# Performance work log

Hardware: AMD Instinct MI355X
Metric: run time of the kernel (lower is better)

The kernel has to match this reference:

```python
import jax, jax.numpy as jnp
import numpy as np

KERNEL_SIZE = 3


def extract_local_features(feature_map, point_coords, kernel_size=KERNEL_SIZE):
    # feature_map: (B,C,H,W); point_coords: (B,N,2) normalized (y,x) in [0,1]
    B, C, H, W = feature_map.shape
    half = kernel_size // 2
    x = (point_coords[..., 1] * (W - 1)).astype(jnp.int32)  # (B,N)
    y = (point_coords[..., 0] * (H - 1)).astype(jnp.int32)
    x_min = jnp.clip(x - half, 0, None)
    x_max = jnp.clip(x + half + 1, None, W)
    y_min = jnp.clip(y - half, 0, None)
    y_max = jnpp_clip = jnp.clip(y + half + 1, None, H)
    y_max = jnp.clip(y + half + 1, None, H)
    # gather a fixed (k,k) window with clamped offsets, mask out-of-window entries
    offs = jnp.arange(kernel_size)  # (k,)
    yy = y_min[..., None] + offs  # (B,N,k) candidate rows
    xx = x_min[..., None] + offs  # (B,N,k)
    y_valid = yy < y_max[..., None]
    x_valid = xx < x_max[..., None]
    yy_c = jnp.clip(yy, 0, H - 1)
    xx_c = jnp.clip(xx, 0, W - 1)
    # flat spatial indices (B,N,k,k)
    flat_idx = yy_c[..., :, None] * W + xx_c[..., None, :]
    valid = (y_valid[..., :, None] & x_valid[..., None, :]).astype(feature_map.dtype)
    fm_flat = feature_map.reshape(B, C, H * W)  # (B,C,HW)

    def per_batch(fm, idx, val):
        # fm: (C,HW); idx,val: (N,k,k)
        g = fm[:, idx.reshape(-1)].reshape(fm.shape[0], *idx.shape)  # (C,N,k,k)
        s = jnp.einsum('cnij,nij->cn', g, val)
        cnt = val.sum(axis=(-1, -2))  # (N,)
        return s / cnt[None, :]

    return jax.vmap(per_batch)(fm_flat, flat_idx, valid)  # (B,C,N)


def point_sample(inp, point_coords):
    # bilinear grid_sample, align_corners=False, coords in [0,1] as (x,y) order
    # per the code: grid = 2*coords - 1; grid_sample uses (x,y) convention
    B, C, H, W = inp.shape
    gx = point_coords[..., 0]  # (B,N) in [0,1]
    gy = point_coords[..., 1]
    # align_corners=False mapping: pix = ((g*2-1)+1)/2 * size - 0.5 = g*size - 0.5
    fx = gx * W - 0.5
    fy = gy * H - 0.5
    x0 = jnp.floor(fx).astype(jnp.int32)
    y0 = jnp.floor(fy).astype(jnp.int32)
    wx = fx - x0
    wy = fy - y0

    def gather(yc, xc):
        inb = ((yc >= 0) & (yc < H) & (xc >= 0) & (xc < W)).astype(inp.dtype)  # (B,N)
        ycc = jnp.clip(yc, 0, H - 1)
        xcc = jnp.clip(xc, 0, W - 1)
        flat = ycc * W + xcc  # (B,N)
        fm = inp.reshape(B, C, H * W)
        g = jax.vmap(lambda f, i: f[:, i])(fm, flat)  # (B,C,N)
        return g * inb[:, None, :]

    v00 = gather(y0, x0)
    v01 = gather(y0, x0 + 1)
    v10 = gather(y0 + 1, x0)
    v11 = gather(y0 + 1, x0 + 1)
    wx_ = wx[:, None, :]
    wy_ = wy[:, None, :]
    out = (v00 * (1 - wx_) * (1 - wy_) + v01 * wx_ * (1 - wy_)
           + v10 * (1 - wx_) * wy_ + v11 * wx_ * wy_)  # (B,C,N)
    return out.transpose(0, 2, 1)  # (B,N,C)


def calculate_uncertainty(mask_logits):
    return -jnp.abs(mask_logits).squeeze(1)  # (B,H,W)


def edge_topk_sampling(edge_masks, uncertainty_map, topk):
    # edge_masks: (B,H,W) {0,1}; uncertainty_map: (B,H,W)
    B, H, W = edge_masks.shape
    NEG = jnp.asarray(-1e30, uncertainty_map.dtype)
    masked_u = jnp.where(edge_masks.reshape(B, -1) == 1,
                         uncertainty_map.reshape(B, -1), NEG)
    vals, idx = jax.lax.top_k(masked_u, topk)  # (B,topk)
    yi = (idx // W).astype(jnp.float32)
    xi = (idx % W).astype(jnp.float32)
    coords = jnp.stack([yi / (H - 1), xi / (W - 1)], axis=-1)  # (B,topk,2) (y,x)
    return idx, coords


def setup_inputs() -> dict:
    key = jax.random.key(0)
    k1, k2, k3, k4 = jax.random.split(key, 4)
    B, C, H, W = 8, 256, 256, 256
    N = 4096
    feature_map = jax.random.normal(k1, (B, C, H, W), dtype=jnp.float32)
    pred_mask = jax.random.normal(k2, (B, 1, H, W), dtype=jnp.float32)
    edge_masks = jax.random.randint(k3, (B, H, W), 0, 2).astype(jnp.int32)
    point_coords = jax.random.uniform(k4, (B, N, 2), dtype=jnp.float32)
    return {"feature_map": feature_map, "pred_mask": pred_mask,
            "edge_masks": edge_masks, "point_coords": point_coords,
            "topk": 4096}


def reference(feature_map, pred_mask, edge_masks, point_coords, topk):
    uncertainty_map = calculate_uncertainty(pred_mask)  # (B,H,W)
    idx, important_coords = edge_topk_sampling(edge_masks, uncertainty_map, topk)
    local_feats = extract_local_features(feature_map, important_coords)  # (B,C,topk)
    sampled = point_sample(feature_map, point_coords)  # (B,N,C)
    return local_feats, sampled, important_coords, idx
```

## Files before the change

### kernel.cpp

```cpp
#include <hip/hip_runtime.h>

#define CC 256
#define HH 256
#define WW 256
#define HWV 65536
#define NN 4096

using u64 = unsigned long long;
using u32 = unsigned int;

__global__ void build_keys_k(const float* __restrict__ pm, const int* __restrict__ em,
                             u64* __restrict__ keys) {
    int i = blockIdx.x * blockDim.x + threadIdx.x;
    float f = (em[i] == 1) ? -fabsf(pm[i]) : -1e30f;
    u32 u = __float_as_uint(f);
    u32 k = (u & 0x80000000u) ? ~u : (u | 0x80000000u);
    u32 pix = (u32)i & 0xFFFFu;
    keys[i] = ((u64)k << 16) | (u64)(0xFFFFu - pix);
}

__global__ __launch_bounds__(1024) void topk_sortpc_k(const u64* __restrict__ keys,
                                                      const float* __restrict__ pc,
                                                      u32* __restrict__ stash,
                                                      u32* __restrict__ pixSorted,
                                                      u32* __restrict__ pcSorted) {
    __shared__ u64 sel[NN];
    __shared__ u64 bm[1024];
    __shared__ u32 wp[1024];
    __shared__ u32 s_digit, s_rem, s_cnt;
    const int t = threadIdx.x;
    if (blockIdx.x < 8) {
        const int b = blockIdx.x;
        const u64* kb = keys + (size_t)b * HWV;
        u32* hist = (u32*)sel;
        u64 prefix = 0ULL;
        u32 remaining = NN;
        for (int r = 0; r < 4; ++r) {
            int shift = 36 - 12 * r;
            #pragma unroll
            for (int q = 0; q < 4; ++q) hist[t + q * 1024] = 0u;
            __syncthreads();
            for (int i = t; i < HWV; i += 1024) {
                u64 K = kb[i];
                if ((K >> (shift + 12)) == prefix)
                    atomicAdd(&hist[(u32)((K >> shift) & 0xFFFULL)], 1u);
            }
            __syncthreads();
            for (int off = 1; off < 4096; off <<= 1) {
                u32 v[4];
                #pragma unroll
                for (int q = 0; q < 4; ++q) {
                    int i = t + q * 1024;
                    v[q] = hist[i];
                    if (i + off < 4096) v[q] += hist[i + off];
                }
                __syncthreads();
                #pragma unroll
                for (int q = 0; q < 4; ++q) hist[t + q * 1024] = v[q];
                __syncthreads();
            }
            #pragma unroll
            for (int q = 0; q < 4; ++q) {
                int d = t + q * 1024;
                u32 ge = hist[d];
                u32 gt = (d < 4095) ? hist[d + 1] : 0u;
                if (ge >= remaining && gt < remaining) { s_digit = (u32)d; s_rem = remaining - gt; }
            }
            __syncthreads();
            prefix = (prefix << 12) | (u64)s_digit;
            remaining = s_rem;
            __syncthreads();
        }
        if (t == 0) s_cnt = 0u;
        __syncthreads();
        for (int i = t; i < HWV; i += 1024) {
            u64 K = kb[i];
            if (K >= prefix) { u32 p = atomicAdd(&s_cnt, 1u); sel[p] = K; }
        }
        __syncthreads();
        for (int k = 2; k <= NN; k <<= 1) {
            for (int j = k >> 1; j > 0; j >>= 1) {
                for (int i = t; i < NN; i += 1024) {
                    int l = i ^ j;
                    if (l > i) {
                        u64 a = sel[i], c = sel[l];
                        bool asc = ((i & k) == 0);
                        if ((a < c) == asc) { sel[i] = c; sel[l] = a; }
                    }
                }
                __syncthreads();
            }
        }
        bm[t] = 0ULL;
        __syncthreads();
        #pragma unroll
        for (int q = 0; q < 4; ++q) {
            int r = t + q * 1024;
            u32 pix = 0xFFFFu - (u32)(sel[r] & 0xFFFFULL);
            stash[b * NN + r] = pix;
            atomicOr(&bm[pix >> 6], 1ULL << (pix & 63));
        }
        __syncthreads();
        wp[t] = (u32)__popcll(bm[t]);
        __syncthreads();
        for (int off = 1; off < 1024; off <<= 1) {
            u32 v = wp[t];
            if (t >= off) v += wp[t - off];
            __syncthreads();
            wp[t] = v;
            __syncthreads();
        }
        #pragma unroll
        for (int q = 0; q < 4; ++q) {
            int r = t + q * 1024;
            u32 pix = 0xFFFFu - (u32)(sel[r] & 0xFFFFULL);
            int w = (int)(pix >> 6);
            u32 pos = wp[w] - (u32)__popcll(bm[w])
                    + (u32)__popcll(bm[w] & ((1ULL << (pix & 63)) - 1ULL));
            pixSorted[b * NN + pos] = (pix << 12) | (u32)r;
        }
    } else {
        const int b = blockIdx.x - 8;
        u32* cellArr = (u32*)sel;
        u32* hist256 = wp;
        u32* cnt     = (u32*)bm;
        if (t < 256) { hist256[t] = 0u; cnt[t] = 0u; }
        __syncthreads();
        for (int n = t; n < NN; n += 1024) {
            float gx = pc[((size_t)b * NN + n) * 2 + 0];
            float gy = pc[((size_t)b * NN + n) * 2 + 1];
            float fx = gx * 256.0f - 0.5f;
            float fy = gy * 256.0f - 0.5f;
            int x0 = (int)floorf(fx), y0 = (int)floorf(fy);
            int xc = min(max(x0, 0), 255), yc = min(max(y0, 0), 255);
            cellArr[n] = ((u32)(yc * 256 + xc) << 12) | (u32)n;
            atomicAdd(&hist256[yc], 1u);
        }
        __syncthreads();
        for (int off = 1; off < 256; off <<= 1) {
            u32 v = 0;
            if (t < 256) { v = hist256[t]; if (t >= off) v += hist256[t - off]; }
            __syncthreads();
            if (t < 256) hist256[t] = v;
            __syncthreads();
        }
        for (int n = t; n < NN; n += 1024) {
            u32 pk = cellArr[n];
            u32 yc = pk >> 20;
            u32 base = (yc > 0) ? hist256[yc - 1] : 0u;
            u32 pos = base + atomicAdd(&cnt[yc], 1u);
            pcSorted[b * NN + pos] = pk;
        }
    }
}

template<int MODE>
__global__ __launch_bounds__(256) void gather_k(const float* __restrict__ fm,
                                                const float* __restrict__ pc,
                                                const u32* __restrict__ pixSorted,
                                                const u32* __restrict__ pcSorted,
                                                float* __restrict__ outLp,
                                                float* __restrict__ outS) {
    __shared__ float tile[256][33];
    __shared__ u32 pidx[256];
    const int b = blockIdx.z, j0 = blockIdx.x * 256, t = threadIdx.x;
    bool doL; int c0;
    if (MODE == 0) { doL = (blockIdx.y < 8); c0 = (doL ? blockIdx.y : blockIdx.y - 8) * 32; }
    else if (MODE == 1) { doL = true; c0 = blockIdx.y * 32; }
    else { doL = false; c0 = blockIdx.y * 32; }
    const float* planes = fm + ((size_t)b * CC + c0) * HWV;

    if (doL) {
        u32 packed = pixSorted[b * NN + j0 + t];
        u32 pix = packed >> 12;
        pidx[t] = packed & 0xFFFu;
        int yi = (int)(pix >> 8), xi = (int)(pix & 255u);
        float cy = (float)yi / 255.0f;
        float cx = (float)xi / 255.0f;
        int x = (int)(cx * 255.0f);
        int y = (int)(cy * 255.0f);
        int x_min = max(x - 1, 0), x_max = min(x + 2, WW);
        int y_min = max(y - 1, 0), y_max = min(y + 2, HH);
        int xb = min(x_min, WW - 4);
        float w0 = (xb + 0 >= x_min && xb + 0 < x_max) ? 1.0f : 0.0f;
        float w1 = (xb + 1 >= x_min && xb + 1 < x_max) ? 1.0f : 0.0f;
        float w2 = (xb + 2 >= x_min && xb + 2 < x_max) ? 1.0f : 0.0f;
        float w3 = (xb + 3 >= x_min && xb + 3 < x_max) ? 1.0f : 0.0f;
        float wr2 = (y_min + 2 < y_max) ? 1.0f : 0.0f;
        int o0 = y_min * WW + xb;
        int o1 = o0 + WW;
        int o2 = min(y_min + 2, HH - 1) * WW + xb;
        float invc = 1.0f / (float)((x_max - x_min) * (y_max - y_min));
        #pragma unroll 4
        for (int j = 0; j < 32; ++j) {
            const float* p = planes + (size_t)j * HWV;
            float s0 = p[o0] * w0 + p[o0 + 1] * w1 + p[o0 + 2] * w2 + p[o0 + 3] * w3;
            float s1 = p[o1] * w0 + p[o1 + 1] * w1 + p[o1 + 2] * w2 + p[o1 + 3] * w3;
            float s2 = p[o2] * w0 + p[o2 + 1] * w1 + p[o2 + 2] * w2 + p[o2 + 3] * w3;
            tile[t][j] = (s0 + s1 + wr2 * s2) * invc;
        }
        __syncthreads();
        for (int idx = t; idx < 8192; idx += 256) {
            int p = idx >> 5, k = idx & 31;
            outLp[((size_t)b * NN + pidx[p]) * CC + c0 + k] = tile[p][k];
        }
    } else {
        int n = (int)(pcSorted[b * NN + j0 + t] & 0xFFFu);
        pidx[t] = (u32)n;
        float gx = pc[((size_t)b * NN + n) * 2 + 0];
        float gy = pc[((size_t)b * NN + n) * 2 + 1];
        float fx = gx * 256.0f - 0.5f;
        float fy = gy * 256.0f - 0.5f;
        float fx0 = floorf(fx), fy0 = floorf(fy);
        int x0 = (int)fx0, y0 = (int)fy0;
        float wx = fx - fx0, wy = fy - fy0;
        int xb = min(max(x0, 0), WW - 2);
        float wv0, wv1;
        if (x0 < 0)            { wv0 = wx;        wv1 = 0.0f; }
        else if (x0 >= WW - 1) { wv0 = 0.0f;      wv1 = 1.0f - wx; }
        else                   { wv0 = 1.0f - wx; wv1 = wx; }
        float wr0 = (y0 >= 0)     ? (1.0f - wy) : 0.0f;
        float wr1 = (y0 + 1 < HH) ? wy          : 0.0f;
        int yc0 = min(max(y0, 0), HH - 1);
        int yc1 = min(max(y0 + 1, 0), HH - 1);
        int o0 = yc0 * WW + xb;
        int o1 = yc1 * WW + xb;
        #pragma unroll 4
        for (int j = 0; j < 32; ++j) {
            const float* p = planes + (size_t)j * HWV;
            tile[t][j] = wr0 * (p[o0] * wv0 + p[o0 + 1] * wv1)
                       + wr1 * (p[o1] * wv0 + p[o1 + 1] * wv1);
        }
        __syncthreads();
        for (int idx = t; idx < 8192; idx += 256) {
            int p = idx >> 5, k = idx & 31;
            outS[((size_t)b * NN + pidx[p]) * CC + c0 + k] = tile[p][k];
        }
    }
}

__global__ __launch_bounds__(256) void transpose_k(const float* __restrict__ outLp,
                                                   float* __restrict__ outL) {
    __shared__ float tile[256][33];
    const int b = blockIdx.z, c0 = blockIdx.y * 32, r0 = blockIdx.x * 256;
    const int t = threadIdx.x;
    for (int idx = t; idx < 8192; idx += 256) {
        int p = idx >> 5, k = idx & 31;
        tile[p][k] = outLp[((size_t)b * NN + r0 + p) * CC + c0 + k];
    }
    __syncthreads();
    for (int idx = t; idx < 8192; idx += 256) {
        int cl = idx >> 8, col = idx & 255;
        outL[((size_t)b * CC + c0 + cl) * NN + r0 + col] = tile[col][cl];
    }
}

__global__ void emit_k(const u32* __restrict__ stash, float* __restrict__ outCoord,
                       float* __restrict__ outIdx) {
    int i = blockIdx.x * blockDim.x + threadIdx.x;
    u32 p = stash[i];
    u32 yi = p >> 8, xi = p & 255u;
    outCoord[(size_t)i * 2 + 0] = (float)yi / 255.0f;
    outCoord[(size_t)i * 2 + 1] = (float)xi / 255.0f;
    outIdx[i] = (float)p;
}

extern "C" void kernel_launch(void* const* d_in, const int* in_sizes, int n_in,
                              void* d_out, int out_size, void* d_ws, size_t ws_size,
                              hipStream_t stream) {
    const float* fm = (const float*)d_in[0];
    const float* pm = (const float*)d_in[1];
    const int*   em = (const int*)d_in[2];
    const float* pc = (const float*)d_in[3];
    (void)in_sizes; (void)n_in; (void)out_size;

    float* out      = (float*)d_out;
    float* outL     = out;
    float* outS     = out + (size_t)8388608;
    float* outCoord = out + (size_t)16777216;
    float* outIdx   = out + (size_t)16842752;

    const size_t need_ws = (size_t)40 * 1024 * 1024;
    bool ws_ok = ws_size >= need_ws;

    u64* keys; u32 *stash, *pixSorted, *pcSorted; float* outLp;
    if (ws_ok) {
        char* w = (char*)d_ws;
        keys      = (u64*)w;
        stash     = (u32*)(w + (size_t)4  * 1024 * 1024);
        pixSorted = (u32*)(w + (size_t)4300 * 1024);
        pcSorted  = (u32*)(w + (size_t)4600 * 1024);
        outLp     = (float*)(w + (size_t)5 * 1024 * 1024);
    } else {
        keys      = (u64*)outS;
        stash     = (u32*)outIdx;
        pixSorted = (u32*)outCoord;
        pcSorted  = pixSorted + 32768;
        outLp     = outS;
    }

    hipLaunchKernelGGL(build_keys_k,  dim3(2048), dim3(256),  0, stream, pm, em, keys);
    hipLaunchKernelGGL(topk_sortpc_k, dim3(16),   dim3(1024), 0, stream, keys, pc, stash, pixSorted, pcSorted);
    if (ws_ok) {
        hipLaunchKernelGGL((gather_k<0>), dim3(16, 16, 8), dim3(256), 0, stream,
                           fm, pc, pixSorted, pcSorted, outLp, outS);
        hipLaunchKernelGGL(transpose_k, dim3(16, 8, 8), dim3(256), 0, stream, outLp, outL);
    } else {
        hipLaunchKernelGGL((gather_k<1>), dim3(16, 8, 8), dim3(256), 0, stream,
                           fm, pc, pixSorted, pcSorted, outLp, outS);
        hipLaunchKernelGGL(transpose_k, dim3(16, 8, 8), dim3(256), 0, stream, outLp, outL);
        hipLaunchKernelGGL((gather_k<2>), dim3(16, 8, 8), dim3(256), 0, stream,
                           fm, pc, pixSorted, pcSorted, outS, outS);
    }
    hipLaunchKernelGGL(emit_k, dim3(128), dim3(256), 0, stream, stash, outCoord, outIdx);
}
```

Before: 321.6 us.

## Fuse coord/idx emission into top-k kernel and vectorize local window loads

Result: no change. 324.3 us (+0.9%).

```diff
diff --git a/kernel.cpp b/kernel.cpp
--- a/kernel.cpp
+++ b/kernel.cpp
@@ -19,11 +19,14 @@
     keys[i] = ((u64)k << 16) | (u64)(0xFFFFu - pix);
 }
 
+template<int DIRECT>
 __global__ __launch_bounds__(1024) void topk_sortpc_k(const u64* __restrict__ keys,
                                                       const float* __restrict__ pc,
                                                       u32* __restrict__ stash,
                                                       u32* __restrict__ pixSorted,
-                                                      u32* __restrict__ pcSorted) {
+                                                      u32* __restrict__ pcSorted,
+                                                      float* __restrict__ outCoord,
+                                                      float* __restrict__ outIdx) {
     __shared__ u64 sel[NN];
     __shared__ u64 bm[1024];
     __shared__ u32 wp[1024];
@@ -97,7 +100,14 @@
         for (int q = 0; q < 4; ++q) {
             int r = t + q * 1024;
             u32 pix = 0xFFFFu - (u32)(sel[r] & 0xFFFFULL);
-            stash[b * NN + r] = pix;
+            if (DIRECT) {
+                u32 yi = pix >> 8, xi = pix & 255u;
+                outCoord[((size_t)b * NN + r) * 2 + 0] = (float)yi / 255.0f;
+                outCoord[((size_t)b * NN + r) * 2 + 1] = (float)xi / 255.0f;
+                outIdx[b * NN + r] = (float)pix;
+            } else {
+                stash[b * NN + r] = pix;
+            }
             atomicOr(&bm[pix >> 6], 1ULL << (pix & 63));
         }
         __syncthreads();
@@ -155,12 +165,12 @@
 }
 
 template<int MODE>
-__global__ __launch_bounds__(256) void gather_k(const float* __restrict__ fm,
-                                                const float* __restrict__ pc,
-                                                const u32* __restrict__ pixSorted,
-                                                const u32* __restrict__ pcSorted,
-                                                float* __restrict__ outLp,
-                                                float* __restrict__ outS) {
+__global__ __launch_bounds__(256, 4) void gather_k(const float* __restrict__ fm,
+                                                   const float* __restrict__ pc,
+                                                   const u32* __restrict__ pixSorted,
+                                                   const u32* __restrict__ pcSorted,
+                                                   float* __restrict__ outLp,
+                                                   float* __restrict__ outS) {
     __shared__ float tile[256][33];
     __shared__ u32 pidx[256];
     const int b = blockIdx.z, j0 = blockIdx.x * 256, t = threadIdx.x;
@@ -181,22 +191,31 @@
         int y = (int)(cy * 255.0f);
         int x_min = max(x - 1, 0), x_max = min(x + 2, WW);
         int y_min = max(y - 1, 0), y_max = min(y + 2, HH);
-        int xb = min(x_min, WW - 4);
-        float w0 = (xb + 0 >= x_min && xb + 0 < x_max) ? 1.0f : 0.0f;
-        float w1 = (xb + 1 >= x_min && xb + 1 < x_max) ? 1.0f : 0.0f;
-        float w2 = (xb + 2 >= x_min && xb + 2 < x_max) ? 1.0f : 0.0f;
-        float w3 = (xb + 3 >= x_min && xb + 3 < x_max) ? 1.0f : 0.0f;
+        int base = min(x_min & ~3, WW - 8);
+        float w8[8];
+        #pragma unroll
+        for (int i = 0; i < 8; ++i)
+            w8[i] = (base + i >= x_min && base + i < x_max) ? 1.0f : 0.0f;
         float wr2 = (y_min + 2 < y_max) ? 1.0f : 0.0f;
-        int o0 = y_min * WW + xb;
+        int o0 = y_min * WW + base;
         int o1 = o0 + WW;
-        int o2 = min(y_min + 2, HH - 1) * WW + xb;
+        int o2 = min(y_min + 2, HH - 1) * WW + base;
         float invc = 1.0f / (float)((x_max - x_min) * (y_max - y_min));
-        #pragma unroll 4
+        #pragma unroll 2
         for (int j = 0; j < 32; ++j) {
             const float* p = planes + (size_t)j * HWV;
-            float s0 = p[o0] * w0 + p[o0 + 1] * w1 + p[o0 + 2] * w2 + p[o0 + 3] * w3;
-            float s1 = p[o1] * w0 + p[o1 + 1] * w1 + p[o1 + 2] * w2 + p[o1 + 3] * w3;
-            float s2 = p[o2] * w0 + p[o2 + 1] * w1 + p[o2 + 2] * w2 + p[o2 + 3] * w3;
+            float4 a0 = *(const float4*)(p + o0);
+            float4 b0 = *(const float4*)(p + o0 + 4);
+            float4 a1 = *(const float4*)(p + o1);
+            float4 b1 = *(const float4*)(p + o1 + 4);
+            float4 a2 = *(const float4*)(p + o2);
+            float4 b2 = *(const float4*)(p + o2 + 4);
+            float s0 = a0.x * w8[0] + a0.y * w8[1] + a0.z * w8[2] + a0.w * w8[3]
+                     + b0.x * w8[4] + b0.y * w8[5] + b0.z * w8[6] + b0.w * w8[7];
+            float s1 = a1.x * w8[0] + a1.y * w8[1] + a1.z * w8[2] + a1.w * w8[3]
+                     + b1.x * w8[4] + b1.y * w8[5] + b1.z * w8[6] + b1.w * w8[7];
+            float s2 = a2.x * w8[0] + a2.y * w8[1] + a2.z * w8[2] + a2.w * w8[3]
+                     + b2.x * w8[4] + b2.y * w8[5] + b2.z * w8[6] + b2.w * w8[7];
             tile[t][j] = (s0 + s1 + wr2 * s2) * invc;
         }
         __syncthreads();
@@ -299,18 +318,21 @@
         outLp     = outS;
     }
 
-    hipLaunchKernelGGL(build_keys_k,  dim3(2048), dim3(256),  0, stream, pm, em, keys);
-    hipLaunchKernelGGL(topk_sortpc_k, dim3(16),   dim3(1024), 0, stream, keys, pc, stash, pixSorted, pcSorted);
+    hipLaunchKernelGGL(build_keys_k, dim3(2048), dim3(256), 0, stream, pm, em, keys);
     if (ws_ok) {
+        hipLaunchKernelGGL((topk_sortpc_k<1>), dim3(16), dim3(1024), 0, stream,
+                           keys, pc, stash, pixSorted, pcSorted, outCoord, outIdx);
         hipLaunchKernelGGL((gather_k<0>), dim3(16, 16, 8), dim3(256), 0, stream,
                            fm, pc, pixSorted, pcSorted, outLp, outS);
         hipLaunchKernelGGL(transpose_k, dim3(16, 8, 8), dim3(256), 0, stream, outLp, outL);
     } else {
+        hipLaunchKernelGGL((topk_sortpc_k<0>), dim3(16), dim3(1024), 0, stream,
+                           keys, pc, stash, pixSorted, pcSorted, outCoord, outIdx);
         hipLaunchKernelGGL((gather_k<1>), dim3(16, 8, 8), dim3(256), 0, stream,
                            fm, pc, pixSorted, pcSorted, outLp, outS);
         hipLaunchKernelGGL(transpose_k, dim3(16, 8, 8), dim3(256), 0, stream, outLp, outL);
         hipLaunchKernelGGL((gather_k<2>), dim3(16, 8, 8), dim3(256), 0, stream,
                            fm, pc, pixSorted, pcSorted, outS, outS);
-    }
-    hipLaunchKernelGGL(emit_k, dim3(128), dim3(256), 0, stream, stash, outCoord, outIdx);
-}
+        hipLaunchKernelGGL(emit_k, dim3(128), dim3(256), 0, stream, stash, outCoord, outIdx);
+    }
+}
```
